# Optimization experiments

Measured on AMD Instinct MI355X. Metric: run time of the kernel, lower is better.

Reference implementation:

```python
import jax, jax.numpy as jnp
import numpy as np
from jax import lax

D_MODEL = 512
D_INNER = 1024   # expand=2
D_STATE = 16
D_CONV = 4
DT_RANK = 32     # ceil(d_model/16)
D_FFN = 2048
EPS = 1e-6


def _layernorm(x, g, b):
    mu = jnp.mean(x, axis=-1, keepdims=True)
    var = jnp.mean((x - mu) ** 2, axis=-1, keepdims=True)
    return (x - mu) * lax.rsqrt(var + EPS) * g + b


def _mamba(x, in_w, conv_w, conv_b, xproj_w, dt_w, dt_b, A_log, D_vec, out_w):
    # x: [B, L, d_model]
    B, L, _ = x.shape
    xz = jnp.einsum('bld,ed->ble', x, in_w)           # [B, L, 2*d_inner]
    xc, z = xz[..., :D_INNER], xz[..., D_INNER:]
    # causal depthwise conv over time
    xt = xc.transpose(0, 2, 1)                        # [B, d_inner, L]
    kern = conv_w[:, None, :]                         # [d_inner, 1, d_conv]
    xt = lax.conv_general_dilated(xt, kern, (1,), [(D_CONV - 1, 0)],
                                  feature_group_count=D_INNER)
    xc = jax.nn.silu(xt.transpose(0, 2, 1) + conv_b)  # [B, L, d_inner]
    # input-dependent SSM parameters
    x_dbl = jnp.einsum('bld,ed->ble', xc, xproj_w)    # [B, L, dt_rank+2*d_state]
    dt = x_dbl[..., :DT_RANK]
    Bm = x_dbl[..., DT_RANK:DT_RANK + D_STATE]
    Cm = x_dbl[..., DT_RANK + D_STATE:]
    delta = jax.nn.softplus(jnp.einsum('blr,dr->bld', dt, dt_w) + dt_b)  # [B, L, d_inner]
    A = -jnp.exp(A_log)                               # [d_inner, d_state]

    def step(h, inp):
        d_t, u_t, b_t, c_t = inp                      # [B,di],[B,di],[B,ds],[B,ds]
        dA = jnp.exp(d_t[:, :, None] * A)             # [B, di, ds]
        dBu = (d_t * u_t)[:, :, None] * b_t[:, None, :]
        h = dA * h + dBu
        y = jnp.einsum('bds,bs->bd', h, c_t)
        return h, y

    h0 = jnp.zeros((B, D_INNER, D_STATE), x.dtype)
    xs = (delta.transpose(1, 0, 2), xc.transpose(1, 0, 2),
          Bm.transpose(1, 0, 2), Cm.transpose(1, 0, 2))
    _, ys = lax.scan(step, h0, xs)                    # [L, B, d_inner]
    y = ys.transpose(1, 0, 2) + xc * D_vec
    y = y * jax.nn.silu(z)
    return jnp.einsum('ble,de->bld', y, out_w)        # [B, L, d_model]


def setup_inputs() -> dict:
    key = jax.random.key(0)
    ks = iter(jax.random.split(key, 40))
    B, S, T = 8, 512, 1024

    def nrm(shape, scale=0.02):
        return jax.random.normal(next(ks), shape, dtype=jnp.float32) * scale

    def mamba_params(prefix):
        A_log = jnp.log(jnp.broadcast_to(jnp.arange(1, D_STATE + 1, dtype=jnp.float32),
                                         (D_INNER, D_STATE)))
        return {
            prefix + '_in_w': nrm((2 * D_INNER, D_MODEL)),
            prefix + '_conv_w': nrm((D_INNER, D_CONV), 0.1),
            prefix + '_conv_b': jnp.zeros((D_INNER,), jnp.float32),
            prefix + '_xproj_w': nrm((DT_RANK + 2 * D_STATE, D_INNER)),
            prefix + '_dt_w': nrm((D_INNER, DT_RANK), 0.1),
            prefix + '_dt_b': jnp.full((D_INNER,), -4.0, jnp.float32),
            prefix + '_A_log': A_log,
            prefix + '_D_vec': jnp.ones((D_INNER,), jnp.float32),
            prefix + '_out_w': nrm((D_MODEL, D_INNER)),
        }

    inp = {
        'tgt': jax.random.normal(next(ks), (B, S, D_MODEL), dtype=jnp.float32),
        'memory': jax.random.normal(next(ks), (B, T, D_MODEL), dtype=jnp.float32),
    }
    inp.update(mamba_params('self'))
    inp.update(mamba_params('cross'))
    inp.update({
        'ln1_g': jnp.ones((D_MODEL,), jnp.float32), 'ln1_b': jnp.zeros((D_MODEL,), jnp.float32),
        'ln2_g': jnp.ones((D_MODEL,), jnp.float32), 'ln2_b': jnp.zeros((D_MODEL,), jnp.float32),
        'ln3_g': jnp.ones((D_MODEL,), jnp.float32), 'ln3_b': jnp.zeros((D_MODEL,), jnp.float32),
        'ffn_w1': nrm((D_FFN, D_MODEL)), 'ffn_b1': jnp.zeros((D_FFN,), jnp.float32),
        'ffn_w2': nrm((D_MODEL, D_FFN)), 'ffn_b2': jnp.zeros((D_MODEL,), jnp.float32),
    })
    return inp


def reference(tgt, memory,
              self_in_w, self_conv_w, self_conv_b, self_xproj_w, self_dt_w, self_dt_b,
              self_A_log, self_D_vec, self_out_w,
              cross_in_w, cross_conv_w, cross_conv_b, cross_xproj_w, cross_dt_w, cross_dt_b,
              cross_A_log, cross_D_vec, cross_out_w,
              ln1_g, ln1_b, ln2_g, ln2_b, ln3_g, ln3_b,
              ffn_w1, ffn_b1, ffn_w2, ffn_b2):
    S = tgt.shape[1]
    # self-Mamba block (post-norm, dropout=0)
    t2 = _mamba(tgt, self_in_w, self_conv_w, self_conv_b, self_xproj_w,
                self_dt_w, self_dt_b, self_A_log, self_D_vec, self_out_w)
    t = _layernorm(tgt + t2, ln1_g, ln1_b)
    # cross-Mamba: scan over [memory; tgt], keep last S steps
    cat = jnp.concatenate([memory, t], axis=1)
    c2 = _mamba(cat, cross_in_w, cross_conv_w, cross_conv_b, cross_xproj_w,
                cross_dt_w, cross_dt_b, cross_A_log, cross_D_vec, cross_out_w)[:, -S:]
    t = _layernorm(t + c2, ln2_g, ln2_b)
    # positionwise FFN
    f = jnp.einsum('bld,fd->blf', t, ffn_w1) + ffn_b1
    f = jax.nn.relu(f)
    f = jnp.einsum('blf,df->bld', f, ffn_w2) + ffn_b2
    t = _layernorm(t + f, ln3_g, ln3_b)
    return t
```

## Files before the change

kernel.cpp:

```cpp
#include <hip/hip_runtime.h>
#include <math.h>

#define DM    512
#define DI    1024
#define DSN   16
#define DTR   32
#define DFFN  2048
#define BB    8
#define SS    512
#define TTM   1024
#define LCAT  1536
#define NC    64
#define CONV_R 8

#define ACT_NONE     0
#define ACT_RELU     1
#define ACT_DELTA    3
#define ACT_XDBL     4

typedef __attribute__((ext_vector_type(8))) short short8;
typedef __attribute__((ext_vector_type(8))) unsigned short ushort8;
typedef __attribute__((ext_vector_type(4))) float f32x4;

#define L2E 1.4426950408889634f

__device__ __forceinline__ unsigned short f2b(float f) {
    unsigned int u = __float_as_uint(f);
    return (unsigned short)((u + 0x7FFFu + ((u >> 16) & 1u)) >> 16);
}
__device__ __forceinline__ float b2f(unsigned short h) {
    return __uint_as_float(((unsigned int)h) << 16);
}
__device__ __forceinline__ float fast_softplus(float v) {
    return (v > 20.f) ? v : __logf(1.f + __expf(v));
}
__device__ __forceinline__ float fexp2(float x) {
#if __has_builtin(__builtin_amdgcn_exp2f)
    return __builtin_amdgcn_exp2f(x);
#else
    float r; asm("v_exp_f32 %0, %1" : "=v"(r) : "v"(x)); return r;
#endif
}
__device__ __forceinline__ float frcp(float x) {
    return __builtin_amdgcn_rcpf(x);
}
__device__ __forceinline__ void gld16(const void* g, void* l) {
    __builtin_amdgcn_global_load_lds(
        (const __attribute__((address_space(1))) void*)g,
        (__attribute__((address_space(3))) void*)l, 16, 0, 0);
}

__device__ __forceinline__ int map_row(int m, int mb, int bs, int ro) {
    int q = m / mb;
    return q * bs + ro + (m - q * mb);
}

__global__ __launch_bounds__(256) void mgemm_kernel(
    const unsigned short* __restrict__ A, int mb, int bs, int ro,
    const unsigned short* __restrict__ W, const float* __restrict__ bias,
    float* __restrict__ Cf, unsigned short* __restrict__ Cb,
    float* __restrict__ C2, float* __restrict__ Cf2,
    int N, int K, int act,
    int omb, int obs, int oro, int ldc, int nofs)
{
    __shared__ __align__(16) unsigned short As[128 * 64];
    __shared__ __align__(16) unsigned short Bs[128 * 64];
    int tid = threadIdx.x;
    int lane = tid & 63, wave = tid >> 6;
    int wy = wave >> 1, wx = wave & 1;
    int nx = gridDim.x;
    int f = blockIdx.y * nx + blockIdx.x;
    int xcd = f & 7, j2 = f >> 3;
    int bandh = gridDim.y >> 3;
    int m0 = (xcd * bandh + j2 / nx) * 128;
    int n0 = (j2 % nx) * 128;
    int Kh = K / gridDim.z;
    int kbeg = blockIdx.z * Kh, kend = kbeg + Kh;
    float* Cfo = Cf;
    const float* biaso = bias;
    if (blockIdx.z) { Cfo = Cf2; biaso = nullptr; }

    const unsigned short* ga[4];
    const unsigned short* gb[4];
    unsigned short* la[4];
    unsigned short* lb[4];
    #pragma unroll
    for (int j = 0; j < 4; j++) {
        int c  = wave * 256 + j * 64 + lane;
        int r  = c >> 3;
        int q  = c & 7;
        int g  = q ^ (r & 7);
        int arow = map_row(m0 + r, mb, bs, ro);
        ga[j] = A + (size_t)arow * K + g * 8;
        gb[j] = W + (size_t)(n0 + r) * K + g * 8;
        la[j] = As + (size_t)(wave * 256 + j * 64) * 8;
        lb[j] = Bs + (size_t)(wave * 256 + j * 64) * 8;
    }
    int fm = lane & 15, fg = lane >> 4;
    int sw = fg ^ (fm & 3);
    int b2 = (fm >> 2) & 1;
    const unsigned short* arp = As + ((size_t)(wy * 64 + fm) * 8 + sw) * 8;
    const unsigned short* brp = Bs + ((size_t)(wx * 64 + fm) * 8 + sw) * 8;

    f32x4 acc[4][4];
    #pragma unroll
    for (int i = 0; i < 4; i++)
        #pragma unroll
        for (int j = 0; j < 4; j++) acc[i][j] = 0.f;

    for (int k0 = kbeg; k0 < kend; k0 += 64) {
        #pragma unroll
        for (int j = 0; j < 4; j++) {
            gld16(ga[j] + k0, la[j]);
            gld16(gb[j] + k0, lb[j]);
        }
        __syncthreads();
        #pragma unroll
        for (int h = 0; h < 2; h++) {
            int ho = ((h ^ b2) * 32);
            short8 af[4], bfr[4];
            #pragma unroll
            for (int t = 0; t < 4; t++) af[t]  = *(const short8*)(arp + ho + t * 1024);
            #pragma unroll
            for (int t = 0; t < 4; t++) bfr[t] = *(const short8*)(brp + ho + t * 1024);
            #pragma unroll
            for (int i = 0; i < 4; i++)
                #pragma unroll
                for (int j = 0; j < 4; j++)
                    acc[i][j] = __builtin_amdgcn_mfma_f32_16x16x32_bf16(af[i], bfr[j], acc[i][j], 0, 0, 0);
        }
        __syncthreads();
    }

    int en = lane & 15, em = (lane >> 4) * 4;
    if (act == ACT_XDBL) {
        size_t zb = (size_t)blockIdx.z * omb;
        #pragma unroll
        for (int j = 0; j < 4; j++) {
            int n = n0 + wx * 64 + j * 16 + en;
            if (n >= 64) continue;
            #pragma unroll
            for (int i = 0; i < 4; i++) {
                int mbase = m0 + wy * 64 + i * 16 + em;
                #pragma unroll
                for (int r = 0; r < 4; r++)
                    C2[(zb + mbase + r) * 64 + n] = acc[i][j][r];
            }
        }
        return;
    }
    if (act == ACT_DELTA) {
        #pragma unroll
        for (int j = 0; j < 4; j++) {
            int n = n0 + wx * 64 + j * 16 + en;
            float bv = bias[n];
            #pragma unroll
            for (int i = 0; i < 4; i++) {
                int mbase = m0 + wy * 64 + i * 16 + em;
                #pragma unroll
                for (int r = 0; r < 4; r++) {
                    float v = acc[i][j][r] + bv;
                    Cb[(size_t)(mbase + r) * 1024 + n] = f2b(fast_softplus(v));
                }
            }
        }
        return;
    }
    #pragma unroll
    for (int j = 0; j < 4; j++) {
        int n = n0 + wx * 64 + j * 16 + en;
        float bv = biaso ? biaso[n] : 0.f;
        #pragma unroll
        for (int i = 0; i < 4; i++) {
            int mbase = m0 + wy * 64 + i * 16 + em;
            #pragma unroll
            for (int r = 0; r < 4; r++) {
                float v = acc[i][j][r] + bv;
                if (act == ACT_RELU) v = v > 0.f ? v : 0.f;
                int orow = map_row(mbase + r, omb, obs, oro);
                size_t off = (size_t)orow * ldc + nofs + n;
                if (Cb) Cb[off] = f2b(v);
                else    Cfo[off] = v;
            }
        }
    }
}

__global__ __launch_bounds__(256) void xdbl_combine(
    const float* __restrict__ pxd, unsigned short* __restrict__ dtb,
    float* __restrict__ bcout, int M, int Z)
{
    int idx = blockIdx.x * 256 + threadIdx.x;
    int m = idx >> 4, n4 = idx & 15;
    int n = n4 * 4;
    float4 s = make_float4(0.f, 0.f, 0.f, 0.f);
    for (int z = 0; z < Z; z++) {
        float4 p = *(const float4*)(pxd + ((size_t)z * M + m) * 64 + n);
        s.x += p.x; s.y += p.y; s.z += p.z; s.w += p.w;
    }
    if (n < 32) {
        ((ushort4*)(dtb + (size_t)m * 64))[n4] =
            make_ushort4(f2b(s.x), f2b(s.y), f2b(s.z), f2b(s.w));
    } else {
        *(float4*)(bcout + (size_t)m * 32 + (n - 32)) = s;
        ((ushort4*)(dtb + (size_t)m * 64))[n4] = make_ushort4(0, 0, 0, 0);
    }
}

struct PrepPtrs {
    const float* tgt; const float* mem;
    const float* w[6];
    const float* xpj_s; const float* xpj_c;
    const float* dtw_s; const float* dtw_c;
    unsigned short* tgtb; unsigned short* catb; unsigned short* wb;
    unsigned short* xprojb_s; unsigned short* xprojb_c;
    unsigned short* dtwb_s; unsigned short* dtwb_c;
};
__global__ __launch_bounds__(256) void prep_kernel(PrepPtrs p)
{
    int u = blockIdx.x * 256 + threadIdx.x;
    if (u < 524288) {
        float4 v = ((const float4*)p.tgt)[u];
        ((ushort4*)p.tgtb)[u] = make_ushort4(f2b(v.x), f2b(v.y), f2b(v.z), f2b(v.w));
        return;
    }
    if (u < 1572864) {
        int f = u - 524288;
        int b = f >> 17, rem = f & 131071;
        float4 v = ((const float4*)p.mem)[f];
        ((ushort4*)p.catb)[(size_t)b * 196608 + rem] =
            make_ushort4(f2b(v.x), f2b(v.y), f2b(v.z), f2b(v.w));
        return;
    }
    if (u < 2883584) {
        const int cum[7] = {0, 262144, 524288, 655360, 786432, 1048576, 1310720};
        int i = u - 1572864;
        int seg = 0;
        #pragma unroll
        for (int s = 1; s < 6; s++) seg += (i >= cum[s]);
        float4 v = ((const float4*)p.w[seg])[i - cum[seg]];
        ((ushort4*)p.wb)[i] = make_ushort4(f2b(v.x), f2b(v.y), f2b(v.z), f2b(v.w));
        return;
    }
    if (u < 2949120) {
        int i = u - 2883584;
        const float* src = p.xpj_s;
        unsigned short* dst = p.xprojb_s;
        if (i >= 32768) { i -= 32768; src = p.xpj_c; dst = p.xprojb_c; }
        int n = i >> 8;
        ushort4 o = make_ushort4(0, 0, 0, 0);
        if (n < 64) {
            float4 v = ((const float4*)src)[i];
            o = make_ushort4(f2b(v.x), f2b(v.y), f2b(v.z), f2b(v.w));
        }
        ((ushort4*)dst)[i] = o;
        return;
    }
    {
        int i = u - 2949120;
        const float* src = p.dtw_s;
        unsigned short* dst = p.dtwb_s;
        if (i >= 16384) { i -= 16384; src = p.dtw_c; dst = p.dtwb_c; }
        int n = i >> 4, c = (i & 15) * 4;
        ushort4 o = make_ushort4(0, 0, 0, 0);
        if (c < 32) {
            float4 v = *(const float4*)(src + n * 32 + c);
            o = make_ushort4(f2b(v.x), f2b(v.y), f2b(v.z), f2b(v.w));
        }
        ((ushort4*)dst)[i] = o;
    }
}

__global__ __launch_bounds__(256) void conv_silu_kernel(
    const unsigned short* __restrict__ xz,
    const float* __restrict__ cw,
    const float* __restrict__ cb,
    unsigned short* __restrict__ xc, int L, int total)
{
    int idx = blockIdx.x * blockDim.x + threadIdx.x;
    if (idx >= total) return;
    int d8 = idx & 127;
    int d0 = d8 * 8;
    int t  = idx >> 7;
    int nq = L / CONV_R;
    int b  = t / nq;
    int l0 = (t - b * nq) * CONV_R;
    size_t rbase = (size_t)b * L + l0;

    float4 wv[8];
    #pragma unroll
    for (int j = 0; j < 8; j++) wv[j] = *(const float4*)(cw + (d0 + j) * 4);
    float bias[8];
    {
        float4 c0 = ((const float4*)(cb + d0))[0];
        float4 c1 = ((const float4*)(cb + d0))[1];
        bias[0]=c0.x; bias[1]=c0.y; bias[2]=c0.z; bias[3]=c0.w;
        bias[4]=c1.x; bias[5]=c1.y; bias[6]=c1.z; bias[7]=c1.w;
    }
    ushort8 win[CONV_R + 3];
    #pragma unroll
    for (int k = 0; k < 3; k++) {
        ushort8 z;
        #pragma unroll
        for (int j = 0; j < 8; j++) z[j] = 0;
        win[k] = (l0 - 3 + k >= 0)
            ? *(const ushort8*)(xz + (rbase - 3 + k) * 2048 + d0) : z;
    }
    #pragma unroll
    for (int i = 0; i < CONV_R; i++)
        win[3 + i] = *(const ushort8*)(xz + (rbase + i) * 2048 + d0);

    const float* w = (const float*)&wv[0];
    #pragma unroll
    for (int i = 0; i < CONV_R; i++) {
        float acc[8];
        #pragma unroll
        for (int j = 0; j < 8; j++) acc[j] = bias[j];
        #pragma unroll
        for (int k = 0; k < 4; k++) {
            ushort8 v = win[i + k];
            #pragma unroll
            for (int j = 0; j < 8; j++)
                acc[j] = fmaf(b2f(v[j]), w[j * 4 + k], acc[j]);
        }
        ushort8 o;
        #pragma unroll
        for (int j = 0; j < 8; j++)
            o[j] = f2b(acc[j] * frcp(1.f + __expf(-acc[j])));
        *(ushort8*)(xc + (rbase + i) * 1024 + d0) = o;
    }
}

__global__ __launch_bounds__(256) void scan_part1(
    const unsigned short* __restrict__ delta, const unsigned short* __restrict__ xc,
    const float* __restrict__ bc, const float* __restrict__ A_log,
    float* __restrict__ part_h, float* __restrict__ part_s, int L, int CH)
{
    int tid = threadIdx.x;
    int dblk = blockIdx.x & 3;
    int c    = (blockIdx.x >> 2) & (NC - 1);
    int b    = blockIdx.x / (4 * NC);
    int d    = dblk * 256 + tid;
    float A2[DSN];
    {
        const float4* ap = (const float4*)(A_log + d * DSN);
        #pragma unroll
        for (int q = 0; q < 4; q++) {
            float4 a4 = ap[q];
            A2[q*4+0] = -__expf(a4.x) * L2E;
            A2[q*4+1] = -__expf(a4.y) * L2E;
            A2[q*4+2] = -__expf(a4.z) * L2E;
            A2[q*4+3] = -__expf(a4.w) * L2E;
        }
    }
    float h[DSN];
    #pragma unroll
    for (int s = 0; s < DSN; s++) h[s] = 0.f;
    float ssum = 0.f;
    int l0 = c * CH;
    for (int l = l0; l < l0 + CH; l++) {
        size_t r = (size_t)b * L + l;
        float4 bq[4];
        const float4* bp = (const float4*)(bc + r * 32);
        #pragma unroll
        for (int q = 0; q < 4; q++) bq[q] = bp[q];
        const float* Bm = (const float*)&bq[0];
        float dl = b2f(delta[r * DI + d]);
        float u  = b2f(xc[r * DI + d]);
        float du = dl * u;
        ssum += dl;
        #pragma unroll
        for (int s = 0; s < DSN; s++)
            h[s] = fmaf(fexp2(dl * A2[s]), h[s], du * Bm[s]);
    }
    size_t base = ((size_t)(b * NC + c) * DI + d) * DSN;
    #pragma unroll
    for (int q = 0; q < 4; q++)
        ((float4*)(part_h + base))[q] = make_float4(h[q*4], h[q*4+1], h[q*4+2], h[q*4+3]);
    part_s[(size_t)(b * NC + c) * DI + d] = ssum;
}

__global__ __launch_bounds__(256) void scan_combine(
    const float* __restrict__ A_log,
    float* __restrict__ part_h, const float* __restrict__ part_s)
{
    int idx = blockIdx.x * 256 + threadIdx.x;
    int s  = idx & (DSN - 1);
    int dd = (idx >> 4) & (DI - 1);
    int b  = idx >> 14;
    float A2 = -__expf(A_log[dd * DSN + s]) * L2E;
    float h = 0.f;
    size_t sbase = (size_t)b * NC * DI + dd;
    size_t hbase = ((size_t)b * NC * DI + dd) * DSN + s;
    for (int c = 0; c < NC; c++) {
        float ph = part_h[hbase];
        float S  = part_s[sbase];
        part_h[hbase] = h;
        h = fmaf(fexp2(A2 * S), h, ph);
        hbase += (size_t)DI * DSN;
        sbase += DI;
    }
}

__global__ __launch_bounds__(256) void scan_part2(
    const unsigned short* __restrict__ delta, const unsigned short* __restrict__ xc,
    const float* __restrict__ bc, const unsigned short* __restrict__ xz,
    const float* __restrict__ A_log, const float* __restrict__ Dv,
    const float* __restrict__ part_h,
    unsigned short* __restrict__ out, int L, int CH, int c0, int lmin)
{
    int tid = threadIdx.x;
    int dblk = blockIdx.x & 3;
    int rest = blockIdx.x >> 2;
    int ncp  = NC - c0;
    int c    = c0 + rest % ncp;
    int b    = rest / ncp;
    int d    = dblk * 256 + tid;
    float A2[DSN];
    {
        const float4* ap = (const float4*)(A_log + d * DSN);
        #pragma unroll
        for (int q = 0; q < 4; q++) {
            float4 a4 = ap[q];
            A2[q*4+0] = -__expf(a4.x) * L2E;
            A2[q*4+1] = -__expf(a4.y) * L2E;
            A2[q*4+2] = -__expf(a4.z) * L2E;
            A2[q*4+3] = -__expf(a4.w) * L2E;
        }
    }
    float Dvd = Dv[d];
    size_t base = ((size_t)(b * NC + c) * DI + d) * DSN;
    float h4[4][4];
    #pragma unroll
    for (int q = 0; q < 4; q++) *((float4*)h4[q]) = ((const float4*)(part_h + base))[q];
    float h[DSN];
    #pragma unroll
    for (int s = 0; s < DSN; s++) h[s] = h4[s >> 2][s & 3];
    int l0 = c * CH;
    for (int l = l0; l < l0 + CH; l++) {
        size_t r = (size_t)b * L + l;
        float4 bq[8];
        const float4* bp = (const float4*)(bc + r * 32);
        #pragma unroll
        for (int q = 0; q < 8; q++) bq[q] = bp[q];
        const float* Bm = (const float*)&bq[0];
        const float* Cm = Bm + DSN;
        float dl = b2f(delta[r * DI + d]);
        float u  = b2f(xc[r * DI + d]);
        float du = dl * u;
        float y = 0.f;
        #pragma unroll
        for (int s = 0; s < DSN; s++) {
            h[s] = fmaf(fexp2(dl * A2[s]), h[s], du * Bm[s]);
            y = fmaf(h[s], Cm[s], y);
        }
        if (l >= lmin) {
            float z = b2f(xz[r * 2048 + DI + d]);
            float sil = z * frcp(1.f + __expf(-z));
            out[r * DI + d] = f2b((y + u * Dvd) * sil);
        }
    }
}

__global__ __launch_bounds__(128) void addln_kernel(
    const float* __restrict__ a, int amb, int absd, int aro, int lda,
    const float* __restrict__ bsrc, const float* __restrict__ bsrc2,
    const float* __restrict__ g, const float* __restrict__ be,
    float* __restrict__ outf, int omb, int obsd, int oro, int ldo,
    unsigned short* __restrict__ outb, int bmb, int bbsd, int bro, int ldb)
{
    int m = blockIdx.x, t = threadIdx.x;
    int ar = map_row(m, amb, absd, aro);
    float4 x4 = ((const float4*)(a + (size_t)ar * lda))[t];
    float4 y4 = ((const float4*)(bsrc + (size_t)m * DM))[t];
    float v[4] = {x4.x + y4.x, x4.y + y4.y, x4.z + y4.z, x4.w + y4.w};
    if (bsrc2) {
        float4 z4 = ((const float4*)(bsrc2 + (size_t)m * DM))[t];
        v[0] += z4.x; v[1] += z4.y; v[2] += z4.z; v[3] += z4.w;
    }
    float sum = v[0] + v[1] + v[2] + v[3];
    float sq  = v[0]*v[0] + v[1]*v[1] + v[2]*v[2] + v[3]*v[3];
    #pragma unroll
    for (int o = 32; o > 0; o >>= 1) {
        sum += __shfl_down(sum, o);
        sq  += __shfl_down(sq, o);
    }
    __shared__ float s0[2], s1[2];
    if ((t & 63) == 0) { s0[t >> 6] = sum; s1[t >> 6] = sq; }
    __syncthreads();
    float tot = s0[0] + s0[1];
    float tsq = s1[0] + s1[1];
    float mu = tot * (1.f / DM);
    float var = tsq * (1.f / DM) - mu * mu;
    float rs = rsqrtf(var + 1e-6f);
    float4 g4 = ((const float4*)g)[t];
    float4 b4 = ((const float4*)be)[t];
    float o0 = (v[0] - mu) * rs * g4.x + b4.x;
    float o1 = (v[1] - mu) * rs * g4.y + b4.y;
    float o2 = (v[2] - mu) * rs * g4.z + b4.z;
    float o3 = (v[3] - mu) * rs * g4.w + b4.w;
    if (outf) {
        int orow = map_row(m, omb, obsd, oro);
        ((float4*)(outf + (size_t)orow * ldo))[t] = make_float4(o0, o1, o2, o3);
    }
    if (outb) {
        int brow = map_row(m, bmb, bbsd, bro);
        ((ushort4*)(outb + (size_t)brow * ldb))[t] =
            make_ushort4(f2b(o0), f2b(o1), f2b(o2), f2b(o3));
    }
}

static void run_scan(const unsigned short* dltb, const unsigned short* xcb, const float* bc,
                     const unsigned short* xzb, const float* A_log, const float* Dv,
                     float* part_h, float* part_s, unsigned short* out, int L,
                     int c0, int lmin, hipStream_t stream)
{
    int CH = L / NC;
    int blocks1 = BB * NC * (DI / 256);
    scan_part1<<<blocks1, 256, 0, stream>>>(dltb, xcb, bc, A_log, part_h, part_s, L, CH);
    scan_combine<<<BB * DI * DSN / 256, 256, 0, stream>>>(A_log, part_h, part_s);
    int blocks2 = BB * (NC - c0) * (DI / 256);
    scan_part2<<<blocks2, 256, 0, stream>>>(dltb, xcb, bc, xzb, A_log, Dv, part_h, out, L, CH, c0, lmin);
}

extern "C" void kernel_launch(void* const* d_in, const int* in_sizes, int n_in,
                              void* d_out, int out_size, void* d_ws, size_t ws_size,
                              hipStream_t stream)
{
    const float* tgt       = (const float*)d_in[0];
    const float* memory    = (const float*)d_in[1];
    const float* s_in_w    = (const float*)d_in[2];
    const float* s_conv_w  = (const float*)d_in[3];
    const float* s_conv_b  = (const float*)d_in[4];
    const float* s_xproj_w = (const float*)d_in[5];
    const float* s_dt_w    = (const float*)d_in[6];
    const float* s_dt_b    = (const float*)d_in[7];
    const float* s_A_log   = (const float*)d_in[8];
    const float* s_D_vec   = (const float*)d_in[9];
    const float* s_out_w   = (const float*)d_in[10];
    const float* c_in_w    = (const float*)d_in[11];
    const float* c_conv_w  = (const float*)d_in[12];
    const float* c_conv_b  = (const float*)d_in[13];
    const float* c_xproj_w = (const float*)d_in[14];
    const float* c_dt_w    = (const float*)d_in[15];
    const float* c_dt_b    = (const float*)d_in[16];
    const float* c_A_log   = (const float*)d_in[17];
    const float* c_D_vec   = (const float*)d_in[18];
    const float* c_out_w   = (const float*)d_in[19];
    const float* ln1_g     = (const float*)d_in[20];
    const float* ln1_b     = (const float*)d_in[21];
    const float* ln2_g     = (const float*)d_in[22];
    const float* ln2_b     = (const float*)d_in[23];
    const float* ln3_g     = (const float*)d_in[24];
    const float* ln3_b     = (const float*)d_in[25];
    const float* ffn_w1    = (const float*)d_in[26];
    const float* ffn_b1    = (const float*)d_in[27];
    const float* ffn_w2    = (const float*)d_in[28];
    const float* ffn_b2    = (const float*)d_in[29];
    float* outp = (float*)d_out;

    float* ws     = (float*)d_ws;
    float* bc     = ws;
    float* t1     = bc     + 393216;
    float* tbuf   = t1     + 2097152;
    float* part_h = tbuf   + 2097152;
    float* proj   = part_h;
    float* proj2  = part_h + 2097152;
    float* pxd    = part_h;
    float* part_s = part_h + 8388608;
    unsigned short* ub      = (unsigned short*)(part_s + 524288);
    unsigned short* dltb    = ub;
    unsigned short* catb    = dltb    + 12582912;
    unsigned short* tgtb    = catb    + 6291456;
    unsigned short* xzb     = tgtb    + 2097152;
    unsigned short* xcb     = xzb     + 25165824;
    unsigned short* ygb     = xcb     + 12582912;
    unsigned short* tbbf    = ygb     + 12582912;
    unsigned short* s_in_wb = tbbf    + 2097152;
    unsigned short* c_in_wb = s_in_wb + 1048576;
    unsigned short* s_out_wb= c_in_wb + 1048576;
    unsigned short* c_out_wb= s_out_wb+ 524288;
    unsigned short* w1b     = c_out_wb+ 524288;
    unsigned short* w2b     = w1b     + 1048576;
    unsigned short* xprojb_s= w2b     + 1048576;
    unsigned short* xprojb_c= xprojb_s+ 131072;
    unsigned short* dtwb_s  = xprojb_c+ 131072;
    unsigned short* dtwb_c  = dtwb_s  + 65536;
    unsigned short* dtb     = dtwb_c  + 65536;
    unsigned short* fbuf    = xzb;
    float* ffnout  = (float*)dltb;
    float* ffnout2 = ffnout + 2097152;

    {
        PrepPtrs pp;
        pp.tgt = tgt; pp.mem = memory;
        pp.w[0]=s_in_w; pp.w[1]=c_in_w; pp.w[2]=s_out_w; pp.w[3]=c_out_w; pp.w[4]=ffn_w1; pp.w[5]=ffn_w2;
        pp.xpj_s = s_xproj_w; pp.xpj_c = c_xproj_w;
        pp.dtw_s = s_dt_w;    pp.dtw_c = c_dt_w;
        pp.tgtb = tgtb; pp.catb = catb; pp.wb = s_in_wb;
        pp.xprojb_s = xprojb_s; pp.xprojb_c = xprojb_c;
        pp.dtwb_s = dtwb_s; pp.dtwb_c = dtwb_c;
        prep_kernel<<<11648, 256, 0, stream>>>(pp);
    }

    mgemm_kernel<<<dim3(2048/128, 4096/128), 256, 0, stream>>>(
        tgtb, 4096, 0, 0, s_in_wb, nullptr, nullptr, xzb, nullptr, nullptr, 2048, 512, ACT_NONE,
        4096, 0, 0, 2048, 0);
    conv_silu_kernel<<<(BB*(SS/CONV_R)*128 + 255)/256, 256, 0, stream>>>(
        xzb, s_conv_w, s_conv_b, xcb, SS, BB*(SS/CONV_R)*128);
    mgemm_kernel<<<dim3(1, 4096/128, 4), 256, 0, stream>>>(
        xcb, 4096, 0, 0, xprojb_s, nullptr, nullptr, nullptr, pxd, nullptr, 128, 1024, ACT_XDBL,
        4096, 0, 0, 0, 0);
    xdbl_combine<<<4096*16/256, 256, 0, stream>>>(pxd, dtb, bc, 4096, 4);
    mgemm_kernel<<<dim3(1024/128, 4096/128), 256, 0, stream>>>(
        dtb, 4096, 0, 0, dtwb_s, s_dt_b, nullptr, dltb, nullptr, nullptr, 1024, 64, ACT_DELTA,
        4096, 0, 0, 1024, 0);
    run_scan(dltb, xcb, bc, xzb, s_A_log, s_D_vec, part_h, part_s, ygb, SS, 0, 0, stream);
    mgemm_kernel<<<dim3(512/128, 4096/128, 2), 256, 0, stream>>>(
        ygb, 4096, 0, 0, s_out_wb, nullptr, proj, nullptr, nullptr, proj2, 512, 1024, ACT_NONE,
        4096, 0, 0, 512, 0);
    addln_kernel<<<4096, 128, 0, stream>>>(
        tgt, 4096, 0, 0, DM, proj, proj2, ln1_g, ln1_b,
        t1, 4096, 0, 0, DM, catb, 512, 1536, 1024, DM);

    mgemm_kernel<<<dim3(1024/128, 12288/128), 256, 0, stream>>>(
        catb, 12288, 0, 0, c_in_wb, nullptr, nullptr, xzb, nullptr, nullptr, 2048, 512, ACT_NONE,
        12288, 0, 0, 2048, 0);
    mgemm_kernel<<<dim3(1024/128, 4096/128), 256, 0, stream>>>(
        catb, 512, 1536, 1024, c_in_wb + 1024 * 512, nullptr, nullptr, xzb, nullptr, nullptr, 2048, 512, ACT_NONE,
        512, 1536, 1024, 2048, 1024);
    conv_silu_kernel<<<(BB*(LCAT/CONV_R)*128 + 255)/256, 256, 0, stream>>>(
        xzb, c_conv_w, c_conv_b, xcb, LCAT, BB*(LCAT/CONV_R)*128);
    mgemm_kernel<<<dim3(1, 12288/128, 4), 256, 0, stream>>>(
        xcb, 12288, 0, 0, xprojb_c, nullptr, nullptr, nullptr, pxd, nullptr, 128, 1024, ACT_XDBL,
        12288, 0, 0, 0, 0);
    xdbl_combine<<<12288*16/256, 256, 0, stream>>>(pxd, dtb, bc, 12288, 4);
    mgemm_kernel<<<dim3(1024/128, 12288/128), 256, 0, stream>>>(
        dtb, 12288, 0, 0, dtwb_c, c_dt_b, nullptr, dltb, nullptr, nullptr, 1024, 64, ACT_DELTA,
        12288, 0, 0, 1024, 0);
    run_scan(dltb, xcb, bc, xzb, c_A_log, c_D_vec, part_h, part_s, ygb, LCAT, 42, 1024, stream);
    mgemm_kernel<<<dim3(512/128, 4096/128, 2), 256, 0, stream>>>(
        ygb, 512, 1536, 1024, c_out_wb, nullptr, proj, nullptr, nullptr, proj2, 512, 1024, ACT_NONE,
        4096, 0, 0, 512, 0);
    addln_kernel<<<4096, 128, 0, stream>>>(
        t1, 4096, 0, 0, DM, proj, proj2, ln2_g, ln2_b,
        tbuf, 4096, 0, 0, DM, tbbf, 4096, 0, 0, DM);

    mgemm_kernel<<<dim3(2048/128, 4096/128), 256, 0, stream>>>(
        tbbf, 4096, 0, 0, w1b, ffn_b1, nullptr, fbuf, nullptr, nullptr, 2048, 512, ACT_RELU,
        4096, 0, 0, 2048, 0);
    mgemm_kernel<<<dim3(512/128, 4096/128, 2), 256, 0, stream>>>(
        fbuf, 4096, 0, 0, w2b, ffn_b2, ffnout, nullptr, nullptr, ffnout2, 512, 2048, ACT_NONE,
        4096, 0, 0, 512, 0);
    addln_kernel<<<4096, 128, 0, stream>>>(
        tbuf, 4096, 0, 0, DM, ffnout, ffnout2, ln3_g, ln3_b,
        outp, 4096, 0, 0, DM, nullptr, 0, 0, 0, 0);
}
```

Before: 495.9 us.

## Merge cross in-proj GEMMs, raise split-K to four, shrink scan chunk count

Several changes land together. The two cross-Mamba input-projection GEMMs become one launch, with a y-split that switches the row mapping and weight offset. The out-proj and FFN2 GEMMs move from 2-way to 4-way split-K, and addln now sums a variable number of partial buffers. The scan chunk count drops from 64 to 32, and part1 skips the final chunk whose state is never used. GEMM global addressing also moves to 32-bit offsets. Together these aim to cut launch count and raise occupancy, at the cost of more partial-sum traffic and longer sequential chunks in the scan.

After: 498.9 us. No clear change (+0.6%).

```diff
diff --git a/kernel.cpp b/kernel.cpp
--- a/kernel.cpp
+++ b/kernel.cpp
@@ -10,7 +10,6 @@
 #define SS    512
 #define TTM   1024
 #define LCAT  1536
-#define NC    64
 #define CONV_R 8
 
 #define ACT_NONE     0
@@ -61,27 +60,37 @@
     float* __restrict__ Cf, unsigned short* __restrict__ Cb,
     float* __restrict__ C2, float* __restrict__ Cf2,
     int N, int K, int act,
-    int omb, int obs, int oro, int ldc, int nofs)
+    int omb, int obs, int oro, int ldc, int nofs, int pstr,
+    int ysplit, int amb2, int abs2, int aro2, int wofs2,
+    int omb2, int obs2, int oro2, int nofs2)
 {
     __shared__ __align__(16) unsigned short As[128 * 64];
     __shared__ __align__(16) unsigned short Bs[128 * 64];
     int tid = threadIdx.x;
     int lane = tid & 63, wave = tid >> 6;
     int wy = wave >> 1, wx = wave & 1;
-    int nx = gridDim.x;
-    int f = blockIdx.y * nx + blockIdx.x;
+    int bx = blockIdx.x, by = blockIdx.y;
+    int nx = gridDim.x, ny = gridDim.y;
+    const unsigned short* Wp = W;
+    if (ysplit) {
+        if (by >= ysplit) {
+            by -= ysplit; ny = gridDim.y - ysplit;
+            mb = amb2; bs = abs2; ro = aro2; Wp += wofs2;
+            omb = omb2; obs = obs2; oro = oro2; nofs = nofs2;
+        } else ny = ysplit;
+    }
+    int f = by * nx + bx;
     int xcd = f & 7, j2 = f >> 3;
-    int bandh = gridDim.y >> 3;
+    int bandh = ny >> 3;
     int m0 = (xcd * bandh + j2 / nx) * 128;
     int n0 = (j2 % nx) * 128;
     int Kh = K / gridDim.z;
     int kbeg = blockIdx.z * Kh, kend = kbeg + Kh;
     float* Cfo = Cf;
     const float* biaso = bias;
-    if (blockIdx.z) { Cfo = Cf2; biaso = nullptr; }
-
-    const unsigned short* ga[4];
-    const unsigned short* gb[4];
+    if (blockIdx.z) { Cfo = Cf2 + (size_t)(blockIdx.z - 1) * pstr; biaso = nullptr; }
+
+    unsigned aoff[4], boff[4];
     unsigned short* la[4];
     unsigned short* lb[4];
     #pragma unroll
@@ -91,8 +100,8 @@
         int q  = c & 7;
         int g  = q ^ (r & 7);
         int arow = map_row(m0 + r, mb, bs, ro);
-        ga[j] = A + (size_t)arow * K + g * 8;
-        gb[j] = W + (size_t)(n0 + r) * K + g * 8;
+        aoff[j] = (unsigned)(arow * K + g * 8);
+        boff[j] = (unsigned)((n0 + r) * K + g * 8);
         la[j] = As + (size_t)(wave * 256 + j * 64) * 8;
         lb[j] = Bs + (size_t)(wave * 256 + j * 64) * 8;
     }
@@ -111,8 +120,8 @@
     for (int k0 = kbeg; k0 < kend; k0 += 64) {
         #pragma unroll
         for (int j = 0; j < 4; j++) {
-            gld16(ga[j] + k0, la[j]);
-            gld16(gb[j] + k0, lb[j]);
+            gld16(A  + aoff[j] + k0, la[j]);
+            gld16(Wp + boff[j] + k0, lb[j]);
         }
         __syncthreads();
         #pragma unroll
@@ -334,12 +343,14 @@
 __global__ __launch_bounds__(256) void scan_part1(
     const unsigned short* __restrict__ delta, const unsigned short* __restrict__ xc,
     const float* __restrict__ bc, const float* __restrict__ A_log,
-    float* __restrict__ part_h, float* __restrict__ part_s, int L, int CH)
+    float* __restrict__ part_h, float* __restrict__ part_s, int L, int CH, int NCr)
 {
     int tid = threadIdx.x;
     int dblk = blockIdx.x & 3;
-    int c    = (blockIdx.x >> 2) & (NC - 1);
-    int b    = blockIdx.x / (4 * NC);
+    int rest = blockIdx.x >> 2;
+    int c    = rest % NCr;
+    int b    = rest / NCr;
+    if (c == NCr - 1) return;
     int d    = dblk * 256 + tid;
     float A2[DSN];
     {
@@ -373,16 +384,16 @@
         for (int s = 0; s < DSN; s++)
             h[s] = fmaf(fexp2(dl * A2[s]), h[s], du * Bm[s]);
     }
-    size_t base = ((size_t)(b * NC + c) * DI + d) * DSN;
+    size_t base = ((size_t)(b * NCr + c) * DI + d) * DSN;
     #pragma unroll
     for (int q = 0; q < 4; q++)
         ((float4*)(part_h + base))[q] = make_float4(h[q*4], h[q*4+1], h[q*4+2], h[q*4+3]);
-    part_s[(size_t)(b * NC + c) * DI + d] = ssum;
+    part_s[(size_t)(b * NCr + c) * DI + d] = ssum;
 }
 
 __global__ __launch_bounds__(256) void scan_combine(
     const float* __restrict__ A_log,
-    float* __restrict__ part_h, const float* __restrict__ part_s)
+    float* __restrict__ part_h, const float* __restrict__ part_s, int NCr)
 {
     int idx = blockIdx.x * 256 + threadIdx.x;
     int s  = idx & (DSN - 1);
@@ -390,9 +401,9 @@
     int b  = idx >> 14;
     float A2 = -__expf(A_log[dd * DSN + s]) * L2E;
     float h = 0.f;
-    size_t sbase = (size_t)b * NC * DI + dd;
-    size_t hbase = ((size_t)b * NC * DI + dd) * DSN + s;
-    for (int c = 0; c < NC; c++) {
+    size_t sbase = (size_t)b * NCr * DI + dd;
+    size_t hbase = ((size_t)b * NCr * DI + dd) * DSN + s;
+    for (int c = 0; c < NCr; c++) {
         float ph = part_h[hbase];
         float S  = part_s[sbase];
         part_h[hbase] = h;
@@ -407,12 +418,12 @@
     const float* __restrict__ bc, const unsigned short* __restrict__ xz,
     const float* __restrict__ A_log, const float* __restrict__ Dv,
     const float* __restrict__ part_h,
-    unsigned short* __restrict__ out, int L, int CH, int c0, int lmin)
+    unsigned short* __restrict__ out, int L, int CH, int NCr, int c0, int lmin)
 {
     int tid = threadIdx.x;
     int dblk = blockIdx.x & 3;
     int rest = blockIdx.x >> 2;
-    int ncp  = NC - c0;
+    int ncp  = NCr - c0;
     int c    = c0 + rest % ncp;
     int b    = rest / ncp;
     int d    = dblk * 256 + tid;
@@ -429,7 +440,7 @@
         }
     }
     float Dvd = Dv[d];
-    size_t base = ((size_t)(b * NC + c) * DI + d) * DSN;
+    size_t base = ((size_t)(b * NCr + c) * DI + d) * DSN;
     float h4[4][4];
     #pragma unroll
     for (int q = 0; q < 4; q++) *((float4*)h4[q]) = ((const float4*)(part_h + base))[q];
@@ -464,7 +475,7 @@
 
 __global__ __launch_bounds__(128) void addln_kernel(
     const float* __restrict__ a, int amb, int absd, int aro, int lda,
-    const float* __restrict__ bsrc, const float* __restrict__ bsrc2,
+    const float* __restrict__ bsrc, const float* __restrict__ parts, int nparts, int pstr,
     const float* __restrict__ g, const float* __restrict__ be,
     float* __restrict__ outf, int omb, int obsd, int oro, int ldo,
     unsigned short* __restrict__ outb, int bmb, int bbsd, int bro, int ldb)
@@ -474,8 +485,8 @@
     float4 x4 = ((const float4*)(a + (size_t)ar * lda))[t];
     float4 y4 = ((const float4*)(bsrc + (size_t)m * DM))[t];
     float v[4] = {x4.x + y4.x, x4.y + y4.y, x4.z + y4.z, x4.w + y4.w};
-    if (bsrc2) {
-        float4 z4 = ((const float4*)(bsrc2 + (size_t)m * DM))[t];
+    for (int p = 0; p < nparts; p++) {
+        float4 z4 = ((const float4*)(parts + (size_t)p * pstr + (size_t)m * DM))[t];
         v[0] += z4.x; v[1] += z4.y; v[2] += z4.z; v[3] += z4.w;
     }
     float sum = v[0] + v[1] + v[2] + v[3];
@@ -512,15 +523,15 @@
 
 static void run_scan(const unsigned short* dltb, const unsigned short* xcb, const float* bc,
                      const unsigned short* xzb, const float* A_log, const float* Dv,
-                     float* part_h, float* part_s, unsigned short* out, int L,
+                     float* part_h, float* part_s, unsigned short* out, int L, int NCr,
                      int c0, int lmin, hipStream_t stream)
 {
-    int CH = L / NC;
-    int blocks1 = BB * NC * (DI / 256);
-    scan_part1<<<blocks1, 256, 0, stream>>>(dltb, xcb, bc, A_log, part_h, part_s, L, CH);
-    scan_combine<<<BB * DI * DSN / 256, 256, 0, stream>>>(A_log, part_h, part_s);
-    int blocks2 = BB * (NC - c0) * (DI / 256);
-    scan_part2<<<blocks2, 256, 0, stream>>>(dltb, xcb, bc, xzb, A_log, Dv, part_h, out, L, CH, c0, lmin);
+    int CH = L / NCr;
+    int blocks1 = BB * NCr * (DI / 256);
+    scan_part1<<<blocks1, 256, 0, stream>>>(dltb, xcb, bc, A_log, part_h, part_s, L, CH, NCr);
+    scan_combine<<<BB * DI * DSN / 256, 256, 0, stream>>>(A_log, part_h, part_s, NCr);
+    int blocks2 = BB * (NCr - c0) * (DI / 256);
+    scan_part2<<<blocks2, 256, 0, stream>>>(dltb, xcb, bc, xzb, A_log, Dv, part_h, out, L, CH, NCr, c0, lmin);
 }
 
 extern "C" void kernel_launch(void* const* d_in, const int* in_sizes, int n_in,
@@ -565,7 +576,7 @@
     float* tbuf   = t1     + 2097152;
     float* part_h = tbuf   + 2097152;
     float* proj   = part_h;
-    float* proj2  = part_h + 2097152;
+    float* pparts = part_h + 2097152;
     float* pxd    = part_h;
     float* part_s = part_h + 8388608;
     unsigned short* ub      = (unsigned short*)(part_s + 524288);
@@ -589,7 +600,7 @@
     unsigned short* dtb     = dtwb_c  + 65536;
     unsigned short* fbuf    = xzb;
     float* ffnout  = (float*)dltb;
-    float* ffnout2 = ffnout + 2097152;
+    float* fparts  = ffnout + 2097152;
 
     {
         PrepPtrs pp;
@@ -605,54 +616,52 @@
 
     mgemm_kernel<<<dim3(2048/128, 4096/128), 256, 0, stream>>>(
         tgtb, 4096, 0, 0, s_in_wb, nullptr, nullptr, xzb, nullptr, nullptr, 2048, 512, ACT_NONE,
-        4096, 0, 0, 2048, 0);
+        4096, 0, 0, 2048, 0, 0,  0, 0,0,0, 0, 0,0,0, 0);
     conv_silu_kernel<<<(BB*(SS/CONV_R)*128 + 255)/256, 256, 0, stream>>>(
         xzb, s_conv_w, s_conv_b, xcb, SS, BB*(SS/CONV_R)*128);
     mgemm_kernel<<<dim3(1, 4096/128, 4), 256, 0, stream>>>(
         xcb, 4096, 0, 0, xprojb_s, nullptr, nullptr, nullptr, pxd, nullptr, 128, 1024, ACT_XDBL,
-        4096, 0, 0, 0, 0);
+        4096, 0, 0, 0, 0, 0,  0, 0,0,0, 0, 0,0,0, 0);
     xdbl_combine<<<4096*16/256, 256, 0, stream>>>(pxd, dtb, bc, 4096, 4);
     mgemm_kernel<<<dim3(1024/128, 4096/128), 256, 0, stream>>>(
         dtb, 4096, 0, 0, dtwb_s, s_dt_b, nullptr, dltb, nullptr, nullptr, 1024, 64, ACT_DELTA,
-        4096, 0, 0, 1024, 0);
-    run_scan(dltb, xcb, bc, xzb, s_A_log, s_D_vec, part_h, part_s, ygb, SS, 0, 0, stream);
-    mgemm_kernel<<<dim3(512/128, 4096/128, 2), 256, 0, stream>>>(
-        ygb, 4096, 0, 0, s_out_wb, nullptr, proj, nullptr, nullptr, proj2, 512, 1024, ACT_NONE,
-        4096, 0, 0, 512, 0);
+        4096, 0, 0, 1024, 0, 0,  0, 0,0,0, 0, 0,0,0, 0);
+    run_scan(dltb, xcb, bc, xzb, s_A_log, s_D_vec, part_h, part_s, ygb, SS, 32, 0, 0, stream);
+    mgemm_kernel<<<dim3(512/128, 4096/128, 4), 256, 0, stream>>>(
+        ygb, 4096, 0, 0, s_out_wb, nullptr, proj, nullptr, nullptr, pparts, 512, 1024, ACT_NONE,
+        4096, 0, 0, 512, 0, 2097152,  0, 0,0,0, 0, 0,0,0, 0);
     addln_kernel<<<4096, 128, 0, stream>>>(
-        tgt, 4096, 0, 0, DM, proj, proj2, ln1_g, ln1_b,
+        tgt, 4096, 0, 0, DM, proj, pparts, 3, 2097152, ln1_g, ln1_b,
         t1, 4096, 0, 0, DM, catb, 512, 1536, 1024, DM);
 
-    mgemm_kernel<<<dim3(1024/128, 12288/128), 256, 0, stream>>>(
+    mgemm_kernel<<<dim3(1024/128, 96 + 32), 256, 0, stream>>>(
         catb, 12288, 0, 0, c_in_wb, nullptr, nullptr, xzb, nullptr, nullptr, 2048, 512, ACT_NONE,
-        12288, 0, 0, 2048, 0);
-    mgemm_kernel<<<dim3(1024/128, 4096/128), 256, 0, stream>>>(
-        catb, 512, 1536, 1024, c_in_wb + 1024 * 512, nullptr, nullptr, xzb, nullptr, nullptr, 2048, 512, ACT_NONE,
-        512, 1536, 1024, 2048, 1024);
+        12288, 0, 0, 2048, 0, 0,
+        96, 512, 1536, 1024, 1024 * 512, 512, 1536, 1024, 1024);
     conv_silu_kernel<<<(BB*(LCAT/CONV_R)*128 + 255)/256, 256, 0, stream>>>(
         xzb, c_conv_w, c_conv_b, xcb, LCAT, BB*(LCAT/CONV_R)*128);
     mgemm_kernel<<<dim3(1, 12288/128, 4), 256, 0, stream>>>(
         xcb, 12288, 0, 0, xprojb_c, nullptr, nullptr, nullptr, pxd, nullptr, 128, 1024, ACT_XDBL,
-        12288, 0, 0, 0, 0);
+        12288, 0, 0, 0, 0, 0,  0, 0,0,0, 0, 0,0,0, 0);
     xdbl_combine<<<12288*16/256, 256, 0, stream>>>(pxd, dtb, bc, 12288, 4);
     mgemm_kernel<<<dim3(1024/128, 12288/128), 256, 0, stream>>>(
         dtb, 12288, 0, 0, dtwb_c, c_dt_b, nullptr, dltb, nullptr, nullptr, 1024, 64, ACT_DELTA,
-        12288, 0, 0, 1024, 0);
-    run_scan(dltb, xcb, bc, xzb, c_A_log, c_D_vec, part_h, part_s, ygb, LCAT, 42, 1024, stream);
-    mgemm_kernel<<<dim3(512/128, 4096/128, 2), 256, 0, stream>>>(
-        ygb, 512, 1536, 1024, c_out_wb, nullptr, proj, nullptr, nullptr, proj2, 512, 1024, ACT_NONE,
-        4096, 0, 0, 512, 0);
+        12288, 0, 0, 1024, 0, 0,  0, 0,0,0, 0, 0,0,0, 0);
+    run_scan(dltb, xcb, bc, xzb, c_A_log, c_D_vec, part_h, part_s, ygb, LCAT, 32, 21, 1024, stream);
+    mgemm_kernel<<<dim3(512/128, 4096/128, 4), 256, 0, stream>>>(
+        ygb, 512, 1536, 1024, c_out_wb, nullptr, proj, nullptr, nullptr, pparts, 512, 1024, ACT_NONE,
+        4096, 0, 0, 512, 0, 2097152,  0, 0,0,0, 0, 0,0,0, 0);
     addln_kernel<<<4096, 128, 0, stream>>>(
-        t1, 4096, 0, 0, DM, proj, proj2, ln2_g, ln2_b,
+        t1, 4096, 0, 0, DM, proj, pparts, 3, 2097152, ln2_g, ln2_b,
         tbuf, 4096, 0, 0, DM, tbbf, 4096, 0, 0, DM);
 
     mgemm_kernel<<<dim3(2048/128, 4096/128), 256, 0, stream>>>(
         tbbf, 4096, 0, 0, w1b, ffn_b1, nullptr, fbuf, nullptr, nullptr, 2048, 512, ACT_RELU,
-        4096, 0, 0, 2048, 0);
-    mgemm_kernel<<<dim3(512/128, 4096/128, 2), 256, 0, stream>>>(
-        fbuf, 4096, 0, 0, w2b, ffn_b2, ffnout, nullptr, nullptr, ffnout2, 512, 2048, ACT_NONE,
-        4096, 0, 0, 512, 0);
+        4096, 0, 0, 2048, 0, 0,  0, 0,0,0, 0, 0,0,0, 0);
+    mgemm_kernel<<<dim3(512/128, 4096/128, 4), 256, 0, stream>>>(
+        fbuf, 4096, 0, 0, w2b, ffn_b2, ffnout, nullptr, nullptr, fparts, 512, 2048, ACT_NONE,
+        4096, 0, 0, 512, 0, 2097152,  0, 0,0,0, 0, 0,0,0, 0);
     addln_kernel<<<4096, 128, 0, stream>>>(
-        tbuf, 4096, 0, 0, DM, ffnout, ffnout2, ln3_g, ln3_b,
+        tbuf, 4096, 0, 0, DM, ffnout, fparts, 3, 2097152, ln3_g, ln3_b,
         outp, 4096, 0, 0, DM, nullptr, 0, 0, 0, 0);
 }
```
